# Kernel tuning notes

Measured on AMD Instinct MI355X. Metric: run time of the kernel, lower is better.

## Reference

```python
import jax, jax.numpy as jnp
import numpy as np

B, N, DM, DE, H, L = 4, 256, 128, 8, 2 and 2, 8  # placeholder, real values below
B, N, DM, DE, H, L = 4, 256, 128, 8, 8, 2
D = DM // H  # per-head dim = 16
INNER = H * D


def setup_inputs() -> dict:
    key = jax.random.key(0)
    ks = jax.random.split(key, 20)
    nodes = jax.random.normal(ks[0], (B, N, DM), dtype=jnp.float32)
    edges = jax.random.normal(ks[1], (B, N, N, DE), dtype=jnp.float32)
    adjacency = (jax.random.uniform(ks[2], (B, N, N)) < 0.1).astype(jnp.float32)
    s = 0.02
    p = {
        'Wq': jax.random.normal(ks[3], (L, DM, INNER)) * s,
        'bq': jnp.zeros((L, INNER)),
        'Wk': jax.random.normal(ks[4], (L, DM, INNER)) * s,
        'bk': jnp.zeros((L, INNER)),
        'Wv': jax.random.normal(ks[5], (L, DM, INNER)) * s,
        'bv': jnp.zeros((L, INNER)),
        'We': jax.random.normal(ks[6], (L, DE, INNER)) * s,
        'be': jnp.zeros((L, INNER)),
        'Wres': jax.random.normal(ks[7], (L, DM, DM)) * s,
        'bres': jnp.zeros((L, DM)),
        'Wgate': jax.random.normal(ks[8], (L, 3 * DM, 1)) * s,
        'ln_g': jnp.ones((L, DM)),
        'ln_b': jnp.zeros((L, DM)),
    }
    return {'nodes': nodes, 'edges': edges, 'adjacency': adjacency, **p}


def _adj_softmax(sim, adj):
    # Faithful to source: torch.mean(x, dim, keepdim=True)[0] indexes batch 0,
    # giving a (N,1) shift broadcast over all batch*head rows.
    means = jnp.mean(sim, axis=-1, keepdims=True)[0]
    x_exp = jnp.exp(sim - means) * adj
    s = jnp.sum(x_exp, axis=-1, keepdims=True)
    s = jnp.where(s == 0, 1.0, s)
    return x_exp / s


def reference(nodes, edges, adjacency, Wq, bq, Wk, bk, Wv, bv, We, be,
              Wres, bres, Wgate, ln_g, ln_b):
    b, n, dm = nodes.shape
    h, d = H, DM // H
    scale = 1.0 / jnp.sqrt(jnp.float32(d))
    adj = jnp.broadcast_to(adjacency[:, None], (b, h, n, n)).reshape(b * h, n, n)
    x = nodes
    for l in range(L):  # fixed small layer count
        def heads(t):  # (b,n,h*d) -> (b*h, n, d)
            return t.reshape(b, n, h, d).transpose(0, 2, 1, 3).reshape(b * h, n, d)
        q = heads(x @ Wq[l] + bq[l])
        k = heads(x @ Wk[l] + bk[l])
        v = heads(x @ Wv[l] + bv[l])
        # edge features: (b,n,n,h,d) -> (b*h, n, n, d)
        e = (edges @ We[l] + be[l]).reshape(b, n, n, h, d)
        e = e.transpose(0, 3, 1, 2, 4).reshape(b * h, n, n, d)
        ke = k[:, None, :, :] + e
        ve = v[:, None, :, :] + e
        sim = jnp.einsum('bid,bijd->bij', q, ke) * scale
        attn = _adj_softmax(sim, adj)
        out = jnp.einsum('bij,bijd->bid', attn, ve)
        out = out.reshape(b, h, n, d).transpose(0, 2, 1, 3).reshape(b, n, h * d)
        # GatedResidual
        res = x @ Wres[l] + bres[l]
        gate_in = jnp.concatenate([out, res, out - res], axis=-1)
        g = jax.nn.sigmoid(gate_in @ Wgate[l])
        y = out * g + res * (1 - g)
        mu = jnp.mean(y, axis=-1, keepdims=True)
        var = jnp.var(y, axis=-1, keepdims=True)
        y = (y - mu) / jnp.sqrt(var + 1e-5) * ln_g[l] + ln_b[l]
        x = jax.nn.relu(y)
    return x
```

## Files before the change

kernel.cpp:

```cpp
#include <hip/hip_runtime.h>

#define BB 4
#define NN 256
#define DMM 128
#define DEE 8
#define HH 8
#define DD 16
#define LAYERS 2
#define SCALE 0.25f
#define PS 260
#define SS (BB*NN*DMM)


struct Params {
  const float *nodes, *edges, *adjacency;
  const float *Wq, *bq, *Wk, *bk, *Wv, *bv, *We, *be, *Wres, *bres, *Wgate, *lng, *lnb;
  const float *src;
  float *q, *k, *v, *res;
  float *out;
  int layer;
};

__global__ __launch_bounds__(256) void k_proj(Params P){
  const int t = threadIdx.x;
  const int m = t >> 6;
  const int cp = t & 63;
  const int row0 = blockIdx.x * 2;
  const int l = P.layer;
  const float *W, *bia; float* dst;
  if (m==0){ W = P.Wq + l*DMM*DMM; bia = P.bq + l*DMM; dst = P.q; }
  else if (m==1){ W = P.Wk + l*DMM*DMM; bia = P.bk + l*DMM; dst = P.k; }
  else if (m==2){ W = P.Wv + l*DMM*DMM; bia = P.bv + l*DMM; dst = P.v; }
  else { W = P.Wres + l*DMM*DMM; bia = P.bres + l*DMM; dst = P.res; }
  const float2 bv2 = *(const float2*)(bia + 2*cp);
  float a00=bv2.x, a01=bv2.y, a10=bv2.x, a11=bv2.y;
  const float2* W2 = (const float2*)W;
  const float* xr = P.src + (size_t)row0*DMM;
  #pragma unroll 8
  for (int kk=0; kk<DMM; kk++){
    float2 w = W2[kk*64+cp];
    float x0 = xr[kk], x1 = xr[DMM+kk];
    a00 += x0*w.x; a01 += x0*w.y;
    a10 += x1*w.x; a11 += x1*w.y;
  }
  if (m==1){
    const int b = row0 >> 8, i0 = row0 & 255;
    float* kT = dst + ((size_t)b*DMM + 2*cp)*NN;
    kT[i0]      = a00;  kT[NN + i0]     = a01;
    kT[i0+1]    = a10;  kT[NN + i0+1]   = a11;
  } else {
    *(float2*)(dst + (size_t)row0*DMM     + 2*cp) = make_float2(a00,a01);
    *(float2*)(dst + (size_t)(row0+1)*DMM + 2*cp) = make_float2(a10,a11);
  }
}

__global__ __launch_bounds__(512) void k_mid(Params P){
  const int t = threadIdx.x;
  const int r = t >> 8;
  const int u = t & 255;
  const int row0 = blockIdx.x*2;
  const int row  = row0 + r;
  const int b = row0 >> 8;

  __shared__ float xloc[2][128];
  __shared__ float qs[2][128];
  __shared__ float res_s[2][128];
  __shared__ float qwe_s[2][64];
  __shared__ float qbe_s[2][8];
  __shared__ float es[2][8*PS];
  __shared__ float ps[2][8*PS];
  __shared__ float ssum_s[2][8];
  __shared__ float g_s[2][64];
  __shared__ float red_a[2][2], red_b[2][2], red_c[2][2];

  if (u < 128) qs[r][u]        = P.q  [(size_t)row*DMM + u];
  else         res_s[r][u-128] = P.res[(size_t)row*DMM + (u-128)];
  {
    const int j = u;
    const float4* er4 = (const float4*)(P.edges + ((size_t)row*NN + j)*DEE);
    float4 e0 = er4[0], e1 = er4[1];
    es[r][0*PS+j]=e0.x; es[r][1*PS+j]=e0.y; es[r][2*PS+j]=e0.z; es[r][3*PS+j]=e0.w;
    es[r][4*PS+j]=e1.x; es[r][5*PS+j]=e1.y; es[r][6*PS+j]=e1.z; es[r][7*PS+j]=e1.w;
  }
  __syncthreads();

  if (u < 64){
    const int h = u>>3, c = u&7;
    const float* Wer = P.We + c*DMM + h*DD;
    float a = 0.f;
    #pragma unroll
    for (int d=0; d<DD; d++) a += qs[r][h*DD+d]*Wer[d];
    qwe_s[r][u] = a;
    if (c==0){
      const float* ber = P.be + h*DD;
      float a2=0.f;
      #pragma unroll
      for (int d=0; d<DD; d++) a2 += qs[r][h*DD+d]*ber[d];
      qbe_s[r][h] = a2;
    }
  }
  __syncthreads();

  {
    const int dp = u>>6, jg = u&63;
    const int J = 4*jg;
    const float4 av = *(const float4*)(P.adjacency + (size_t)row*NN + J);
    float hsum[2];
    #pragma unroll
    for (int hh=0; hh<2; hh++){
      const int h = 2*dp+hh;
      float qh[16];
      #pragma unroll
      for (int d=0; d<16; d++) qh[d] = qs[r][h*DD+d];
      float s0=qbe_s[r][h]; float s1=s0, s2=s0, s3=s0;
      const float* kbase = P.k + ((size_t)b*DMM + h*DD)*NN + J;
      #pragma unroll
      for (int db=0; db<2; db++){
        float4 krg[8];
        #pragma unroll
        for (int d=0; d<8; d++) krg[d] = *(const float4*)(kbase + (size_t)(db*8+d)*NN);
        #pragma unroll
        for (int d=0; d<8; d++){
          float qv = qh[db*8+d];
          s0 += qv*krg[d].x; s1 += qv*krg[d].y; s2 += qv*krg[d].z; s3 += qv*krg[d].w;
        }
      }
      #pragma unroll
      for (int c=0; c<8; c++){
        float4 ev = *(const float4*)(&es[r][c*PS + J]);
        float wv = qwe_s[r][h*8+c];
        s0 += wv*ev.x; s1 += wv*ev.y; s2 += wv*ev.z; s3 += wv*ev.w;
      }
      float4 p;
      p.x = __expf(s0*SCALE)*av.x;
      p.y = __expf(s1*SCALE)*av.y;
      p.z = __expf(s2*SCALE)*av.z;
      p.w = __expf(s3*SCALE)*av.w;
      *(float4*)(&ps[r][h*PS + J]) = p;
      hsum[hh] = (p.x+p.y)+(p.z+p.w);
    }
    float v0 = hsum[0], v1 = hsum[1];
    #pragma unroll
    for (int off=32; off; off>>=1){ v0 += __shfl_xor(v0,off,64); v1 += __shfl_xor(v1,off,64); }
    if (jg==0){ ssum_s[r][2*dp] = v0; ssum_s[r][2*dp+1] = v1; }
  }
  __syncthreads();

  float pv = 0.f;
  if (u < 128){
    const int h = u>>4;
    const float* vcol = P.v + (size_t)b*NN*DMM + u;
    const float4* pr = (const float4*)(&ps[r][h*PS]);
    #pragma unroll 4
    for (int jq=0; jq<64; jq++){
      float4 pp = pr[jq];
      const float* vv = vcol + jq*4*DMM;
      pv += pp.x*vv[0] + pp.y*vv[DMM] + pp.z*vv[2*DMM] + pp.w*vv[3*DMM];
    }
  } else if (u < 192){
    const int h=(u-128)>>3, c=(u-128)&7;
    const float4* pr = (const float4*)(&ps[r][h*PS]);
    const float4* er = (const float4*)(&es[r][c*PS]);
    float g=0.f;
    #pragma unroll 4
    for (int jq=0; jq<64; jq++){
      float4 pp=pr[jq], ee=er[jq];
      g += pp.x*ee.x + pp.y*ee.y + pp.z*ee.z + pp.w*ee.w;
    }
    g_s[r][h*8+c]=g;
  }
  __syncthreads();

  float o=0.f, rr=0.f;
  if (u<128){
    const int h = u>>4;
    const float* Wec = P.We + u;
    float eacc=0.f;
    #pragma unroll
    for (int c=0;c<8;c++) eacc += Wec[c*DMM]*g_s[r][h*8+c];
    const float ssum = ssum_s[r][h];
    const float denom = (ssum==0.f)?1.f:ssum;
    const float bev = P.be[u];
    o = (pv + eacc + ssum*bev)/denom;
    rr = res_s[r][u];
    const float* Wg = P.Wgate;
    float contrib = o*Wg[u] + rr*Wg[DMM+u] + (o-rr)*Wg[2*DMM+u];
    #pragma unroll
    for (int off=32; off; off>>=1) contrib += __shfl_xor(contrib, off, 64);
    if ((u&63)==0) red_a[r][u>>6]=contrib;
  }
  __syncthreads();

  float y=0.f;
  if (u<128){
    const float gs = red_a[r][0]+red_a[r][1];
    const float gate = 1.f/(1.f+__expf(-gs));
    y = o*gate + rr*(1.f-gate);
    float s1=y, s2=y*y;
    #pragma unroll
    for (int off=32; off; off>>=1){ s1+=__shfl_xor(s1,off,64); s2+=__shfl_xor(s2,off,64); }
    if ((u&63)==0){ red_b[r][u>>6]=s1; red_c[r][u>>6]=s2; }
  }
  __syncthreads();

  if (u<128){
    const float mu  = (red_b[r][0]+red_b[r][1])*(1.f/128.f);
    const float var = (red_c[r][0]+red_c[r][1])*(1.f/128.f) - mu*mu;
    const float inv = rsqrtf(var+1e-5f);
    float yn = (y-mu)*inv*P.lng[u] + P.lnb[u];
    xloc[r][u] = fmaxf(yn, 0.f);
  }
  __syncthreads();

  {
    const int w = t>>6, m = w&3, ri = w>>2, cp = t&63;
    const float *W, *bia; float* dst;
    if (m==0){ W=P.Wq+DMM*DMM;   bia=P.bq+DMM;   dst=P.q;   }
    else if (m==1){ W=P.Wk+DMM*DMM;   bia=P.bk+DMM;   dst=P.k;   }
    else if (m==2){ W=P.Wv+DMM*DMM;   bia=P.bv+DMM;   dst=P.v;   }
    else          { W=P.Wres+DMM*DMM; bia=P.bres+DMM; dst=P.res; }
    const float2 bv2 = *(const float2*)(bia+2*cp);
    float a0=bv2.x, a1=bv2.y;
    const float2* W2 = (const float2*)W;
    const float* xr = xloc[ri];
    #pragma unroll 8
    for (int kk=0; kk<DMM; kk++){
      float2 w2 = W2[kk*64+cp];
      float xv = xr[kk];
      a0 += xv*w2.x; a1 += xv*w2.y;
    }
    const int prow = row0 + ri;
    if (m==1){
      const int pb = prow >> 8, pi = prow & 255;
      float* kT = dst + SS + ((size_t)pb*DMM + 2*cp)*NN;
      kT[pi] = a0; kT[NN + pi] = a1;
    } else {
      *(float2*)(dst + SS + (size_t)prow*DMM + 2*cp) = make_float2(a0,a1);
    }
  }
}

__global__ __launch_bounds__(256) void k_attn(Params P){
  const int t = threadIdx.x;
  const int b = blockIdx.x >> 8;
  const int i = blockIdx.x & 255;
  const int l = P.layer;

  __shared__ float qs[128];
  __shared__ float qwe_s[64];
  __shared__ float qbe_s[8];
  __shared__ float es[8*PS];
  __shared__ float ps[8*PS];
  __shared__ float ssum_s[8];
  __shared__ float g_s[64];
  __shared__ float res_s[128];
  __shared__ float red_a[2], red_b[2], red_c[2];

  if (t < 128) qs[t] = P.q[(b*NN+i)*DMM + t];
  {
    const int j = t;
    const float4* er4 = (const float4*)(P.edges + ((size_t)(b*NN+i)*NN + j)*DEE);
    float4 e0 = er4[0], e1 = er4[1];
    es[0*PS+j]=e0.x; es[1*PS+j]=e0.y; es[2*PS+j]=e0.z; es[3*PS+j]=e0.w;
    es[4*PS+j]=e1.x; es[5*PS+j]=e1.y; es[6*PS+j]=e1.z; es[7*PS+j]=e1.w;
  }
  __syncthreads();
  if (t < 64){
    const int h = t>>3, c = t&7;
    const float* Wer = P.We + l*DEE*DMM + c*DMM + h*DD;
    float a = 0.f;
    #pragma unroll
    for (int d=0; d<DD; d++) a += qs[h*DD+d]*Wer[d];
    qwe_s[t] = a;
    if (c==0){
      const float* ber = P.be + l*DMM + h*DD;
      float a2 = 0.f;
      #pragma unroll
      for (int d=0; d<DD; d++) a2 += qs[h*DD+d]*ber[d];
      qbe_s[h] = a2;
    }
  }
  __syncthreads();

  {
    const int dp = t>>6, jg = t&63;
    const int J = 4*jg;
    const float4 av = *(const float4*)(P.adjacency + (size_t)(b*NN+i)*NN + J);
    float hsum[2];
    #pragma unroll
    for (int hh=0; hh<2; hh++){
      const int h = 2*dp+hh;
      float qh[16];
      #pragma unroll
      for (int d=0; d<16; d++) qh[d] = qs[h*DD+d];
      float s0=qbe_s[h]; float s1=s0, s2=s0, s3=s0;
      const float* kbase = P.k + ((size_t)b*DMM + h*DD)*NN + J;
      #pragma unroll
      for (int db=0; db<2; db++){
        float4 krg[8];
        #pragma unroll
        for (int d=0; d<8; d++) krg[d] = *(const float4*)(kbase + (size_t)(db*8+d)*NN);
        #pragma unroll
        for (int d=0; d<8; d++){
          float qv = qh[db*8+d];
          s0 += qv*krg[d].x; s1 += qv*krg[d].y; s2 += qv*krg[d].z; s3 += qv*krg[d].w;
        }
      }
      #pragma unroll
      for (int c=0; c<8; c++){
        float4 ev = *(const float4*)(&es[c*PS + J]);
        float wv = qwe_s[h*8+c];
        s0 += wv*ev.x; s1 += wv*ev.y; s2 += wv*ev.z; s3 += wv*ev.w;
      }
      float4 p;
      p.x = __expf(s0*SCALE)*av.x;
      p.y = __expf(s1*SCALE)*av.y;
      p.z = __expf(s2*SCALE)*av.z;
      p.w = __expf(s3*SCALE)*av.w;
      *(float4*)(&ps[h*PS + J]) = p;
      hsum[hh] = (p.x+p.y)+(p.z+p.w);
    }
    float v0 = hsum[0], v1 = hsum[1];
    #pragma unroll
    for (int off=32; off; off>>=1){ v0 += __shfl_xor(v0,off,64); v1 += __shfl_xor(v1,off,64); }
    if (jg==0){ ssum_s[2*dp] = v0; ssum_s[2*dp+1] = v1; }
  }
  __syncthreads();

  float pv = 0.f;
  if (t < 128){
    const int h = t>>4;
    const float* vcol = P.v + b*NN*DMM + t;
    const float4* pr = (const float4*)(ps + h*PS);
    #pragma unroll 4
    for (int jq=0; jq<64; jq++){
      float4 pp = pr[jq];
      const float* vv = vcol + jq*4*DMM;
      pv += pp.x*vv[0] + pp.y*vv[DMM] + pp.z*vv[2*DMM] + pp.w*vv[3*DMM];
    }
  } else if (t < 192){
    const int h = (t-128)>>3, c = (t-128)&7;
    const float4* pr = (const float4*)(ps + h*PS);
    const float4* er = (const float4*)(es + c*PS);
    float g = 0.f;
    #pragma unroll 4
    for (int jq=0; jq<64; jq++){
      float4 pp = pr[jq], ee = er[jq];
      g += pp.x*ee.x + pp.y*ee.y + pp.z*ee.z + pp.w*ee.w;
    }
    g_s[h*8+c] = g;
  } else {
    const int u = t - 192;
    const float2 rv = *(const float2*)(P.res + (b*NN+i)*DMM + 2*u);
    res_s[2*u] = rv.x; res_s[2*u+1] = rv.y;
  }
  __syncthreads();

  float o = 0.f, rr = 0.f;
  if (t < 128){
    const int h = t>>4;
    const float* Wec = P.We + l*DEE*DMM + t;
    float eacc = 0.f;
    #pragma unroll
    for (int c=0;c<8;c++) eacc += Wec[c*DMM] * g_s[h*8+c];
    const float ssum = ssum_s[h];
    const float denom = (ssum==0.f) ? 1.f : ssum;
    const float bev = P.be[l*DMM + t];
    o = (pv + eacc + ssum*bev) / denom;
    rr = res_s[t];
    const float* Wg = P.Wgate + l*3*DMM;
    float contrib = o*Wg[t] + rr*Wg[DMM+t] + (o-rr)*Wg[2*DMM+t];
    #pragma unroll
    for (int off=32; off; off>>=1) contrib += __shfl_xor(contrib, off, 64);
    if ((t&63)==0) red_a[t>>6] = contrib;
  }
  __syncthreads();

  float y = 0.f;
  if (t < 128){
    const float gs = red_a[0] + red_a[1];
    const float gate = 1.f/(1.f + __expf(-gs));
    y = o*gate + rr*(1.f-gate);
    float s1 = y, s2 = y*y;
    #pragma unroll
    for (int off=32; off; off>>=1){ s1 += __shfl_xor(s1, off, 64); s2 += __shfl_xor(s2, off, 64); }
    if ((t&63)==0){ red_b[t>>6] = s1; red_c[t>>6] = s2; }
  }
  __syncthreads();

  if (t < 128){
    const float mu  = (red_b[0]+red_b[1]) * (1.f/128.f);
    const float var = (red_c[0]+red_c[1]) * (1.f/128.f) - mu*mu;
    const float inv = rsqrtf(var + 1e-5f);
    float yn = (y - mu)*inv*P.lng[l*DMM+t] + P.lnb[l*DMM+t];
    yn = fmaxf(yn, 0.f);
    P.out[(b*NN+i)*DMM + t] = yn;
  }
}

extern "C" void kernel_launch(void* const* d_in, const int* in_sizes, int n_in,
                              void* d_out, int out_size, void* d_ws, size_t ws_size,
                              hipStream_t stream) {
  Params P;
  P.nodes     = (const float*)d_in[0];
  P.edges     = (const float*)d_in[1];
  P.adjacency = (const float*)d_in[2];
  P.Wq   = (const float*)d_in[3];  P.bq   = (const float*)d_in[4];
  P.Wk   = (const float*)d_in[5];  P.bk   = (const float*)d_in[6];
  P.Wv   = (const float*)d_in[7];  P.bv   = (const float*)d_in[8];
  P.We   = (const float*)d_in[9];  P.be   = (const float*)d_in[10];
  P.Wres = (const float*)d_in[11]; P.bres = (const float*)d_in[12];
  P.Wgate= (const float*)d_in[13];
  P.lng  = (const float*)d_in[14]; P.lnb  = (const float*)d_in[15];

  float* f = (float*)d_ws;
  float* qbuf = f;
  float* kbuf = f + 2*SS;
  float* vbuf = f + 4*SS;
  float* rbuf = f + 6*SS;
  P.out = (float*)d_out;

  P.layer = 0; P.src = P.nodes;
  P.q = qbuf; P.k = kbuf; P.v = vbuf; P.res = rbuf;
  hipLaunchKernelGGL(k_proj, dim3(BB*NN/2), dim3(256), 0, stream, P);

  hipLaunchKernelGGL(k_mid, dim3(BB*NN/2), dim3(512), 0, stream, P);

  P.layer = 1;
  P.q = qbuf + SS; P.k = kbuf + SS; P.v = vbuf + SS; P.res = rbuf + SS;
  hipLaunchKernelGGL(k_attn, dim3(BB*NN), dim3(256), 0, stream, P);
}
```

Before: 146.8 us.

## Split attention-value and edge-gather reductions across all threads with shuffle combine

The P·V accumulation now uses all 256 threads per row. Each pair of threads sums half of the j range and the halves are combined with a lane shuffle, with the result staged in shared memory. The edge-gather reduction also splits across thread pairs, and the residual load moves to the kernel start. The q·k dot product reads q as float4 from shared memory instead of a per-thread register copy, and launch bounds gain a minimum-blocks hint of 4. This is meant to remove idle threads and shorten the serial reduction loops, at the cost of an extra shuffle, more shared memory and possible register pressure from the occupancy hint.

```diff
diff --git a/kernel.cpp b/kernel.cpp
--- a/kernel.cpp
+++ b/kernel.cpp
@@ -54,7 +54,7 @@
   }
 }
 
-__global__ __launch_bounds__(512) void k_mid(Params P){
+__global__ __launch_bounds__(512, 4) void k_mid(Params P){
   const int t = threadIdx.x;
   const int r = t >> 8;
   const int u = t & 255;
@@ -69,6 +69,7 @@
   __shared__ float qbe_s[2][8];
   __shared__ float es[2][8*PS];
   __shared__ float ps[2][8*PS];
+  __shared__ float pv_s[2][128];
   __shared__ float ssum_s[2][8];
   __shared__ float g_s[2][64];
   __shared__ float red_a[2][2], red_b[2][2], red_c[2][2];
@@ -109,21 +110,23 @@
     #pragma unroll
     for (int hh=0; hh<2; hh++){
       const int h = 2*dp+hh;
-      float qh[16];
-      #pragma unroll
-      for (int d=0; d<16; d++) qh[d] = qs[r][h*DD+d];
       float s0=qbe_s[r][h]; float s1=s0, s2=s0, s3=s0;
       const float* kbase = P.k + ((size_t)b*DMM + h*DD)*NN + J;
       #pragma unroll
       for (int db=0; db<2; db++){
+        float4 qA = *(const float4*)(&qs[r][h*DD+db*8]);
+        float4 qB = *(const float4*)(&qs[r][h*DD+db*8+4]);
         float4 krg[8];
         #pragma unroll
         for (int d=0; d<8; d++) krg[d] = *(const float4*)(kbase + (size_t)(db*8+d)*NN);
-        #pragma unroll
-        for (int d=0; d<8; d++){
-          float qv = qh[db*8+d];
-          s0 += qv*krg[d].x; s1 += qv*krg[d].y; s2 += qv*krg[d].z; s3 += qv*krg[d].w;
-        }
+        s0 += qA.x*krg[0].x + qA.y*krg[1].x + qA.z*krg[2].x + qA.w*krg[3].x
+            + qB.x*krg[4].x + qB.y*krg[5].x + qB.z*krg[6].x + qB.w*krg[7].x;
+        s1 += qA.x*krg[0].y + qA.y*krg[1].y + qA.z*krg[2].y + qA.w*krg[3].y
+            + qB.x*krg[4].y + qB.y*krg[5].y + qB.z*krg[6].y + qB.w*krg[7].y;
+        s2 += qA.x*krg[0].z + qA.y*krg[1].z + qA.z*krg[2].z + qA.w*krg[3].z
+            + qB.x*krg[4].z + qB.y*krg[5].z + qB.z*krg[6].z + qB.w*krg[7].z;
+        s3 += qA.x*krg[0].w + qA.y*krg[1].w + qA.z*krg[2].w + qA.w*krg[3].w
+            + qB.x*krg[4].w + qB.y*krg[5].w + qB.z*krg[6].w + qB.w*krg[7].w;
       }
       #pragma unroll
       for (int c=0; c<8; c++){
@@ -146,28 +149,40 @@
   }
   __syncthreads();
 
-  float pv = 0.f;
+  {
+    const int h = u>>5, d=(u>>1)&15, half=u&1;
+    const int col = h*DD + d;
+    const float* vbase = P.v + (size_t)b*NN*DMM + col + (size_t)half*128*DMM;
+    const float4* pr = (const float4*)(&ps[r][h*PS]) + half*32;
+    float pv = 0.f;
+    for (int c4=0; c4<8; c4++){
+      float4 pp[4]; float vv[16];
+      #pragma unroll
+      for (int q=0; q<4; q++) pp[q] = pr[c4*4+q];
+      #pragma unroll
+      for (int q=0; q<4; q++){
+        const float* vb = vbase + (size_t)(c4*4+q)*4*DMM;
+        vv[4*q+0]=vb[0]; vv[4*q+1]=vb[DMM]; vv[4*q+2]=vb[2*DMM]; vv[4*q+3]=vb[3*DMM];
+      }
+      #pragma unroll
+      for (int q=0; q<4; q++)
+        pv += pp[q].x*vv[4*q] + pp[q].y*vv[4*q+1] + pp[q].z*vv[4*q+2] + pp[q].w*vv[4*q+3];
+    }
+    pv += __shfl_xor(pv, 1, 64);
+    if (!half) pv_s[r][col] = pv;
+  }
   if (u < 128){
-    const int h = u>>4;
-    const float* vcol = P.v + (size_t)b*NN*DMM + u;
-    const float4* pr = (const float4*)(&ps[r][h*PS]);
-    #pragma unroll 4
-    for (int jq=0; jq<64; jq++){
-      float4 pp = pr[jq];
-      const float* vv = vcol + jq*4*DMM;
-      pv += pp.x*vv[0] + pp.y*vv[DMM] + pp.z*vv[2*DMM] + pp.w*vv[3*DMM];
-    }
-  } else if (u < 192){
-    const int h=(u-128)>>3, c=(u-128)&7;
-    const float4* pr = (const float4*)(&ps[r][h*PS]);
-    const float4* er = (const float4*)(&es[r][c*PS]);
+    const int hg=u>>4, cg=(u>>1)&7, halfg=u&1;
+    const float4* pr = (const float4*)(&ps[r][hg*PS]) + halfg*32;
+    const float4* er = (const float4*)(&es[r][cg*PS]) + halfg*32;
     float g=0.f;
     #pragma unroll 4
-    for (int jq=0; jq<64; jq++){
+    for (int jq=0; jq<32; jq++){
       float4 pp=pr[jq], ee=er[jq];
       g += pp.x*ee.x + pp.y*ee.y + pp.z*ee.z + pp.w*ee.w;
     }
-    g_s[r][h*8+c]=g;
+    g += __shfl_xor(g, 1, 64);
+    if (!halfg) g_s[r][hg*8+cg]=g;
   }
   __syncthreads();
 
@@ -181,7 +196,7 @@
     const float ssum = ssum_s[r][h];
     const float denom = (ssum==0.f)?1.f:ssum;
     const float bev = P.be[u];
-    o = (pv + eacc + ssum*bev)/denom;
+    o = (pv_s[r][u] + eacc + ssum*bev)/denom;
     rr = res_s[r][u];
     const float* Wg = P.Wgate;
     float contrib = o*Wg[u] + rr*Wg[DMM+u] + (o-rr)*Wg[2*DMM+u];
@@ -240,7 +255,7 @@
   }
 }
 
-__global__ __launch_bounds__(256) void k_attn(Params P){
+__global__ __launch_bounds__(256, 4) void k_attn(Params P){
   const int t = threadIdx.x;
   const int b = blockIdx.x >> 8;
   const int i = blockIdx.x & 255;
@@ -251,12 +266,14 @@
   __shared__ float qbe_s[8];
   __shared__ float es[8*PS];
   __shared__ float ps[8*PS];
+  __shared__ float pv_s[128];
   __shared__ float ssum_s[8];
   __shared__ float g_s[64];
   __shared__ float res_s[128];
   __shared__ float red_a[2], red_b[2], red_c[2];
 
-  if (t < 128) qs[t] = P.q[(b*NN+i)*DMM + t];
+  if (t < 128) qs[t]        = P.q  [(b*NN+i)*DMM + t];
+  else         res_s[t-128] = P.res[(b*NN+i)*DMM + (t-128)];
   {
     const int j = t;
     const float4* er4 = (const float4*)(P.edges + ((size_t)(b*NN+i)*NN + j)*DEE);
@@ -290,21 +307,23 @@
     #pragma unroll
     for (int hh=0; hh<2; hh++){
       const int h = 2*dp+hh;
-      float qh[16];
-      #pragma unroll
-      for (int d=0; d<16; d++) qh[d] = qs[h*DD+d];
       float s0=qbe_s[h]; float s1=s0, s2=s0, s3=s0;
       const float* kbase = P.k + ((size_t)b*DMM + h*DD)*NN + J;
       #pragma unroll
       for (int db=0; db<2; db++){
+        float4 qA = *(const float4*)(&qs[h*DD+db*8]);
+        float4 qB = *(const float4*)(&qs[h*DD+db*8+4]);
         float4 krg[8];
         #pragma unroll
         for (int d=0; d<8; d++) krg[d] = *(const float4*)(kbase + (size_t)(db*8+d)*NN);
-        #pragma unroll
-        for (int d=0; d<8; d++){
-          float qv = qh[db*8+d];
-          s0 += qv*krg[d].x; s1 += qv*krg[d].y; s2 += qv*krg[d].z; s3 += qv*krg[d].w;
-        }
+        s0 += qA.x*krg[0].x + qA.y*krg[1].x + qA.z*krg[2].x + qA.w*krg[3].x
+            + qB.x*krg[4].x + qB.y*krg[5].x + qB.z*krg[6].x + qB.w*krg[7].x;
+        s1 += qA.x*krg[0].y + qA.y*krg[1].y + qA.z*krg[2].y + qA.w*krg[3].y
+            + qB.x*krg[4].y + qB.y*krg[5].y + qB.z*krg[6].y + qB.w*krg[7].y;
+        s2 += qA.x*krg[0].z + qA.y*krg[1].z + qA.z*krg[2].z + qA.w*krg[3].z
+            + qB.x*krg[4].z + qB.y*krg[5].z + qB.z*krg[6].z + qB.w*krg[7].z;
+        s3 += qA.x*krg[0].w + qA.y*krg[1].w + qA.z*krg[2].w + qA.w*krg[3].w
+            + qB.x*krg[4].w + qB.y*krg[5].w + qB.z*krg[6].w + qB.w*krg[7].w;
       }
       #pragma unroll
       for (int c=0; c<8; c++){
@@ -327,32 +346,40 @@
   }
   __syncthreads();
 
-  float pv = 0.f;
+  {
+    const int h = t>>5, d=(t>>1)&15, half=t&1;
+    const int col = h*DD + d;
+    const float* vbase = P.v + (size_t)b*NN*DMM + col + (size_t)half*128*DMM;
+    const float4* pr = (const float4*)(ps + h*PS) + half*32;
+    float pv = 0.f;
+    for (int c4=0; c4<8; c4++){
+      float4 pp[4]; float vv[16];
+      #pragma unroll
+      for (int q=0; q<4; q++) pp[q] = pr[c4*4+q];
+      #pragma unroll
+      for (int q=0; q<4; q++){
+        const float* vb = vbase + (size_t)(c4*4+q)*4*DMM;
+        vv[4*q+0]=vb[0]; vv[4*q+1]=vb[DMM]; vv[4*q+2]=vb[2*DMM]; vv[4*q+3]=vb[3*DMM];
+      }
+      #pragma unroll
+      for (int q=0; q<4; q++)
+        pv += pp[q].x*vv[4*q] + pp[q].y*vv[4*q+1] + pp[q].z*vv[4*q+2] + pp[q].w*vv[4*q+3];
+    }
+    pv += __shfl_xor(pv, 1, 64);
+    if (!half) pv_s[col] = pv;
+  }
   if (t < 128){
-    const int h = t>>4;
-    const float* vcol = P.v + b*NN*DMM + t;
-    const float4* pr = (const float4*)(ps + h*PS);
+    const int hg=t>>4, cg=(t>>1)&7, halfg=t&1;
+    const float4* pr = (const float4*)(ps + hg*PS) + halfg*32;
+    const float4* er = (const float4*)(es + cg*PS) + halfg*32;
+    float g=0.f;
     #pragma unroll 4
-    for (int jq=0; jq<64; jq++){
-      float4 pp = pr[jq];
-      const float* vv = vcol + jq*4*DMM;
-      pv += pp.x*vv[0] + pp.y*vv[DMM] + pp.z*vv[2*DMM] + pp.w*vv[3*DMM];
-    }
-  } else if (t < 192){
-    const int h = (t-128)>>3, c = (t-128)&7;
-    const float4* pr = (const float4*)(ps + h*PS);
-    const float4* er = (const float4*)(es + c*PS);
-    float g = 0.f;
-    #pragma unroll 4
-    for (int jq=0; jq<64; jq++){
-      float4 pp = pr[jq], ee = er[jq];
+    for (int jq=0; jq<32; jq++){
+      float4 pp=pr[jq], ee=er[jq];
       g += pp.x*ee.x + pp.y*ee.y + pp.z*ee.z + pp.w*ee.w;
     }
-    g_s[h*8+c] = g;
-  } else {
-    const int u = t - 192;
-    const float2 rv = *(const float2*)(P.res + (b*NN+i)*DMM + 2*u);
-    res_s[2*u] = rv.x; res_s[2*u+1] = rv.y;
+    g += __shfl_xor(g, 1, 64);
+    if (!halfg) g_s[hg*8+cg]=g;
   }
   __syncthreads();
 
@@ -366,7 +393,7 @@
     const float ssum = ssum_s[h];
     const float denom = (ssum==0.f) ? 1.f : ssum;
     const float bev = P.be[l*DMM + t];
-    o = (pv + eacc + ssum*bev) / denom;
+    o = (pv_s[t] + eacc + ssum*bev) / denom;
     rr = res_s[t];
     const float* Wg = P.Wgate + l*3*DMM;
     float contrib = o*Wg[t] + rr*Wg[DMM+t] + (o-rr)*Wg[2*DMM+t];
```

Measured after the change: 163.8 us. 1.12x slower.
